# Kernel tuning notes

Hardware: AMD Instinct MI355X
Metric: run time of the kernel (lower is better)

Reference implementation:

```python
import jax, jax.numpy as jnp
import numpy as np


def setup_inputs() -> dict:
    key = jax.random.key(0)
    ks = jax.random.split(key, 5)
    shape = (8, 96, 128, 128)  # (N, C, H, W)
    X = jax.random.normal(ks[0], shape, dtype=jnp.float32)
    B = jax.random.uniform(ks[1], shape, dtype=jnp.float32)
    G1 = jax.random.uniform(ks[2], shape, dtype=jnp.float32)
    G2 = jax.random.uniform(ks[3], shape, dtype=jnp.float32)
    G3 = jax.random.uniform(ks[4], shape, dtype=jnp.float32)
    return {"X": X, "B": B, "G1": G1, "G2": G2, "G3": G3}


def _gaterecurrent(X, B, G1, G2, G3):
    # H[n,c,h,w] = B*X + G1*Hprev[h-1] + G2*Hprev[h] + G3*Hprev[h+1],
    # where Hprev is column w-1; column 0 has no recurrent input.
    # Scan over width; each carry is one column of shape (N, C, H).
    def to_cols(t):
        return jnp.moveaxis(t, -1, 0)  # (W, N, C, H)

    xs = tuple(to_cols(t) for t in (X, B, G1, G2, G3))
    n, c, h, w = X.shape
    h0 = jnp.zeros((n, c, h), dtype=X.dtype)
    zcol = jnp.zeros((n, c, 1), dtype=X.dtype)

    def step(h_prev, cols):
        x, b, g1, g2, g3 = cols
        h_up = jnp.concatenate([zcol, h_prev[..., :-1]], axis=-1)   # H[h-1, w-1]
        h_dn = jnp.concatenate([h_prev[..., 1:], zcol], axis=-1)    # H[h+1, w-1]
        h_new = b * x + g1 * h_up + g2 * h_prev + g3 * h_dn
        return h_new, h_new

    _, cols_out = jax.lax.scan(step, h0, xs)  # (W, N, C, H)
    return jnp.moveaxis(cols_out, 0, -1)      # (N, C, H, W)


def reference(X, B, G1, G2, G3):
    return _gaterecurrent(X, B, G1, G2, G3)
```

## Files before the change

kernel.cpp:

```cpp
#include <hip/hip_runtime.h>

#define HH 128
#define WW 128
#define SW 32

__global__ __launch_bounds__(128, 2) void gr2d_kernel(
    const float* __restrict__ X, const float* __restrict__ Bm,
    const float* __restrict__ G1, const float* __restrict__ G2,
    const float* __restrict__ G3, float* __restrict__ Out)
{
    const int t = threadIdx.x;
    const size_t rb = (size_t)blockIdx.x * (HH * WW) + (size_t)t * WW;

    __shared__ float halo[2][2];
    if (t == 0) { halo[0][0] = 0.f; halo[0][1] = 0.f; }
    __syncthreads();

    float hp = 0.f;

    for (int sw = 0; sw < WW / SW; ++sw) {
        const float* xp = X  + rb + sw * SW;
        const float* bp = Bm + rb + sw * SW;
        const float* ap = G1 + rb + sw * SW;
        const float* cp = G2 + rb + sw * SW;
        const float* dp = G3 + rb + sw * SW;

#define LDJ(p, j) (*reinterpret_cast<const float4*>((p) + 4 * (j)))
        float4 xv0 = LDJ(xp,0), xv1 = LDJ(xp,1), xv2 = LDJ(xp,2), xv3 = LDJ(xp,3),
               xv4 = LDJ(xp,4), xv5 = LDJ(xp,5), xv6 = LDJ(xp,6), xv7 = LDJ(xp,7);
        float4 bv0 = LDJ(bp,0), bv1 = LDJ(bp,1), bv2 = LDJ(bp,2), bv3 = LDJ(bp,3),
               bv4 = LDJ(bp,4), bv5 = LDJ(bp,5), bv6 = LDJ(bp,6), bv7 = LDJ(bp,7);
        float4 av0 = LDJ(ap,0), av1 = LDJ(ap,1), av2 = LDJ(ap,2), av3 = LDJ(ap,3),
               av4 = LDJ(ap,4), av5 = LDJ(ap,5), av6 = LDJ(ap,6), av7 = LDJ(ap,7);
        float4 cv0 = LDJ(cp,0), cv1 = LDJ(cp,1), cv2 = LDJ(cp,2), cv3 = LDJ(cp,3),
               cv4 = LDJ(cp,4), cv5 = LDJ(cp,5), cv6 = LDJ(cp,6), cv7 = LDJ(cp,7);
        float4 dv0 = LDJ(dp,0), dv1 = LDJ(dp,1), dv2 = LDJ(dp,2), dv3 = LDJ(dp,3),
               dv4 = LDJ(dp,4), dv5 = LDJ(dp,5), dv6 = LDJ(dp,6), dv7 = LDJ(dp,7);
        __builtin_amdgcn_sched_barrier(0);

#define MUL4(a, b) a.x *= b.x; a.y *= b.y; a.z *= b.z; a.w *= b.w;
        MUL4(xv0, bv0) MUL4(xv1, bv1) MUL4(xv2, bv2) MUL4(xv3, bv3)
        MUL4(xv4, bv4) MUL4(xv5, bv5) MUL4(xv6, bv6) MUL4(xv7, bv7)

#define STEP(xc, ac, cc, dc, par) do {                                      \
        float up = __shfl_up(hp, 1);                                        \
        float dn = __shfl_down(hp, 1);                                      \
        if (t == 63)  dn = halo[par][1];                                    \
        if (t == 64)  up = halo[par][0];                                    \
        if (t == 0)   up = 0.f;                                             \
        if (t == 127) dn = 0.f;                                             \
        const float h = xc + ac * up + cc * hp + dc * dn;                   \
        if (t == 63) halo[(par) ^ 1][0] = h;                                \
        if (t == 64) halo[(par) ^ 1][1] = h;                                \
        asm volatile("s_waitcnt lgkmcnt(0)" ::: "memory");                  \
        __builtin_amdgcn_s_barrier();                                       \
        hp = h; xc = h;                                                     \
    } while (0)

#define STEP4(v)                                                            \
        STEP(xv##v.x, av##v.x, cv##v.x, dv##v.x, 0);                        \
        STEP(xv##v.y, av##v.y, cv##v.y, dv##v.y, 1);                        \
        STEP(xv##v.z, av##v.z, cv##v.z, dv##v.z, 0);                        \
        STEP(xv##v.w, av##v.w, cv##v.w, dv##v.w, 1);

        STEP4(0) STEP4(1) STEP4(2) STEP4(3)
        STEP4(4) STEP4(5) STEP4(6) STEP4(7)

        float* op = Out + rb + sw * SW;
        *reinterpret_cast<float4*>(op + 0)  = xv0;
        *reinterpret_cast<float4*>(op + 4)  = xv1;
        *reinterpret_cast<float4*>(op + 8)  = xv2;
        *reinterpret_cast<float4*>(op + 12) = xv3;
        *reinterpret_cast<float4*>(op + 16) = xv4;
        *reinterpret_cast<float4*>(op + 20) = xv5;
        *reinterpret_cast<float4*>(op + 24) = xv6;
        *reinterpret_cast<float4*>(op + 28) = xv7;
    }
}

extern "C" void kernel_launch(void* const* d_in, const int* in_sizes, int n_in,
                              void* d_out, int out_size, void* d_ws, size_t ws_size,
                              hipStream_t stream) {
    const float* X  = (const float*)d_in[0];
    const float* Bm = (const float*)d_in[1];
    const float* G1 = (const float*)d_in[2];
    const float* G2 = (const float*)d_in[3];
    const float* G3 = (const float*)d_in[4];
    float* Out = (float*)d_out;

    const int planes = in_sizes[0] / (HH * WW);
    gr2d_kernel<<<dim3(planes), dim3(128), 0, stream>>>(X, Bm, G1, G2, G3, Out);
}
```

Measured before the change: 67.58 us.

## Double-buffer column loads with inline asm to overlap memory with scan

Replaces the sequential 32-column strip loop, which loaded and then scanned each strip, with a software pipeline over 16-column chunks. Two register buffers alternate: the next chunk's loads are issued through inline global_load asm before the current chunk is scanned, and vmcnt waits are counted by hand. The aim is to hide global memory latency behind the barrier-bound serial recurrence. The cost is hand-tracked vmcnt accounting, which is fragile because the stores are interleaved, and more registers held live for two buffers.

```diff
diff --git a/kernel.cpp b/kernel.cpp
--- a/kernel.cpp
+++ b/kernel.cpp
@@ -2,7 +2,68 @@
 
 #define HH 128
 #define WW 128
-#define SW 32
+
+typedef float f4 __attribute__((ext_vector_type(4)));
+
+#define GLOAD(dst, ptr, OFF)                                                  \
+    asm volatile("global_load_dwordx4 %0, %1, off offset:%2"                  \
+                 : "=&v"(dst) : "v"(ptr), "n"(OFF) : "memory");
+
+#define GSTORE(val, ptr, OFF)                                                 \
+    asm volatile("global_store_dwordx4 %0, %1, off offset:%2"                 \
+                 :: "v"(ptr), "v"(val), "n"(OFF) : "memory");
+
+#define VMCNT(N)                                                              \
+    asm volatile("s_waitcnt vmcnt(" #N ")" ::: "memory");                     \
+    __builtin_amdgcn_sched_barrier(0);
+
+#define LD4(P, s, ptr, WOFF)                                                  \
+    GLOAD(P##s##0, ptr, (WOFF)+0)   GLOAD(P##s##1, ptr, (WOFF)+16)            \
+    GLOAD(P##s##2, ptr, (WOFF)+32)  GLOAD(P##s##3, ptr, (WOFF)+48)
+
+#define LD20(P, WOFF)                                                         \
+    LD4(P, x, xp, WOFF) LD4(P, b, bp, WOFF) LD4(P, a, ap, WOFF)               \
+    LD4(P, c, cp, WOFF) LD4(P, d, dp, WOFF)
+
+#define ST4(P, WOFF)                                                          \
+    GSTORE(P##x0, op, (WOFF)+0)   GSTORE(P##x1, op, (WOFF)+16)                \
+    GSTORE(P##x2, op, (WOFF)+32)  GSTORE(P##x3, op, (WOFF)+48)
+
+#define DECLBUF(P)                                                            \
+    f4 P##x0,P##x1,P##x2,P##x3;                                               \
+    f4 P##b0,P##b1,P##b2,P##b3;                                               \
+    f4 P##a0,P##a1,P##a2,P##a3;                                               \
+    f4 P##c0,P##c1,P##c2,P##c3;                                               \
+    f4 P##d0,P##d1,P##d2,P##d3;
+
+#define MUL4(a, b)                                                            \
+    { (a)[0]*=(b)[0]; (a)[1]*=(b)[1]; (a)[2]*=(b)[2]; (a)[3]*=(b)[3]; }
+
+#define FUSE(P)                                                               \
+    MUL4(P##x0,P##b0) MUL4(P##x1,P##b1) MUL4(P##x2,P##b2) MUL4(P##x3,P##b3)
+
+#define STEP(xc, ac, cc, dc, par) do {                                        \
+        float up = __shfl_up(hp, 1);                                          \
+        float dn = __shfl_down(hp, 1);                                        \
+        if (t == 63)  dn = halo[par][1];                                      \
+        if (t == 64)  up = halo[par][0];                                      \
+        if (t == 0)   up = 0.f;                                               \
+        if (t == 127) dn = 0.f;                                               \
+        const float h = (xc) + (ac) * up + (cc) * hp + (dc) * dn;             \
+        if (t == 63) halo[(par) ^ 1][0] = h;                                  \
+        if (t == 64) halo[(par) ^ 1][1] = h;                                  \
+        asm volatile("s_waitcnt lgkmcnt(0)" ::: "memory");                    \
+        __builtin_amdgcn_s_barrier();                                         \
+        hp = h; (xc) = h;                                                     \
+    } while (0)
+
+#define STEP4(P, v)                                                           \
+    STEP(P##x##v[0], P##a##v[0], P##c##v[0], P##d##v[0], 0);                  \
+    STEP(P##x##v[1], P##a##v[1], P##c##v[1], P##d##v[1], 1);                  \
+    STEP(P##x##v[2], P##a##v[2], P##c##v[2], P##d##v[2], 0);                  \
+    STEP(P##x##v[3], P##a##v[3], P##c##v[3], P##d##v[3], 1);
+
+#define SCAN16(P) STEP4(P,0) STEP4(P,1) STEP4(P,2) STEP4(P,3)
 
 __global__ __launch_bounds__(128, 2) void gr2d_kernel(
     const float* __restrict__ X, const float* __restrict__ Bm,
@@ -11,71 +72,33 @@
 {
     const int t = threadIdx.x;
     const size_t rb = (size_t)blockIdx.x * (HH * WW) + (size_t)t * WW;
+    const float* xp = X  + rb;
+    const float* bp = Bm + rb;
+    const float* ap = G1 + rb;
+    const float* cp = G2 + rb;
+    const float* dp = G3 + rb;
+    float*       op = Out + rb;
 
     __shared__ float halo[2][2];
     if (t == 0) { halo[0][0] = 0.f; halo[0][1] = 0.f; }
     __syncthreads();
 
     float hp = 0.f;
+    DECLBUF(A)
+    DECLBUF(B)
 
-    for (int sw = 0; sw < WW / SW; ++sw) {
-        const float* xp = X  + rb + sw * SW;
-        const float* bp = Bm + rb + sw * SW;
-        const float* ap = G1 + rb + sw * SW;
-        const float* cp = G2 + rb + sw * SW;
-        const float* dp = G3 + rb + sw * SW;
+    LD20(A, 0)
 
-#define LDJ(p, j) (*reinterpret_cast<const float4*>((p) + 4 * (j)))
-        float4 xv0 = LDJ(xp,0), xv1 = LDJ(xp,1), xv2 = LDJ(xp,2), xv3 = LDJ(xp,3),
-               xv4 = LDJ(xp,4), xv5 = LDJ(xp,5), xv6 = LDJ(xp,6), xv7 = LDJ(xp,7);
-        float4 bv0 = LDJ(bp,0), bv1 = LDJ(bp,1), bv2 = LDJ(bp,2), bv3 = LDJ(bp,3),
-               bv4 = LDJ(bp,4), bv5 = LDJ(bp,5), bv6 = LDJ(bp,6), bv7 = LDJ(bp,7);
-        float4 av0 = LDJ(ap,0), av1 = LDJ(ap,1), av2 = LDJ(ap,2), av3 = LDJ(ap,3),
-               av4 = LDJ(ap,4), av5 = LDJ(ap,5), av6 = LDJ(ap,6), av7 = LDJ(ap,7);
-        float4 cv0 = LDJ(cp,0), cv1 = LDJ(cp,1), cv2 = LDJ(cp,2), cv3 = LDJ(cp,3),
-               cv4 = LDJ(cp,4), cv5 = LDJ(cp,5), cv6 = LDJ(cp,6), cv7 = LDJ(cp,7);
-        float4 dv0 = LDJ(dp,0), dv1 = LDJ(dp,1), dv2 = LDJ(dp,2), dv3 = LDJ(dp,3),
-               dv4 = LDJ(dp,4), dv5 = LDJ(dp,5), dv6 = LDJ(dp,6), dv7 = LDJ(dp,7);
-        __builtin_amdgcn_sched_barrier(0);
+    VMCNT(0)  LD20(B, 64)   FUSE(A) SCAN16(A) ST4(A, 0)
+    VMCNT(4)  LD20(A, 128)  FUSE(B) SCAN16(B) ST4(B, 64)
+    VMCNT(4)  LD20(B, 192)  FUSE(A) SCAN16(A) ST4(A, 128)
+    VMCNT(4)  LD20(A, 256)  FUSE(B) SCAN16(B) ST4(B, 192)
+    VMCNT(4)  LD20(B, 320)  FUSE(A) SCAN16(A) ST4(A, 256)
+    VMCNT(4)  LD20(A, 384)  FUSE(B) SCAN16(B) ST4(B, 320)
+    VMCNT(4)  LD20(B, 448)  FUSE(A) SCAN16(A) ST4(A, 384)
+    VMCNT(4)  FUSE(B) SCAN16(B) ST4(B, 448)
 
-#define MUL4(a, b) a.x *= b.x; a.y *= b.y; a.z *= b.z; a.w *= b.w;
-        MUL4(xv0, bv0) MUL4(xv1, bv1) MUL4(xv2, bv2) MUL4(xv3, bv3)
-        MUL4(xv4, bv4) MUL4(xv5, bv5) MUL4(xv6, bv6) MUL4(xv7, bv7)
-
-#define STEP(xc, ac, cc, dc, par) do {                                      \
-        float up = __shfl_up(hp, 1);                                        \
-        float dn = __shfl_down(hp, 1);                                      \
-        if (t == 63)  dn = halo[par][1];                                    \
-        if (t == 64)  up = halo[par][0];                                    \
-        if (t == 0)   up = 0.f;                                             \
-        if (t == 127) dn = 0.f;                                             \
-        const float h = xc + ac * up + cc * hp + dc * dn;                   \
-        if (t == 63) halo[(par) ^ 1][0] = h;                                \
-        if (t == 64) halo[(par) ^ 1][1] = h;                                \
-        asm volatile("s_waitcnt lgkmcnt(0)" ::: "memory");                  \
-        __builtin_amdgcn_s_barrier();                                       \
-        hp = h; xc = h;                                                     \
-    } while (0)
-
-#define STEP4(v)                                                            \
-        STEP(xv##v.x, av##v.x, cv##v.x, dv##v.x, 0);                        \
-        STEP(xv##v.y, av##v.y, cv##v.y, dv##v.y, 1);                        \
-        STEP(xv##v.z, av##v.z, cv##v.z, dv##v.z, 0);                        \
-        STEP(xv##v.w, av##v.w, cv##v.w, dv##v.w, 1);
-
-        STEP4(0) STEP4(1) STEP4(2) STEP4(3)
-        STEP4(4) STEP4(5) STEP4(6) STEP4(7)
-
-        float* op = Out + rb + sw * SW;
-        *reinterpret_cast<float4*>(op + 0)  = xv0;
-        *reinterpret_cast<float4*>(op + 4)  = xv1;
-        *reinterpret_cast<float4*>(op + 8)  = xv2;
-        *reinterpret_cast<float4*>(op + 12) = xv3;
-        *reinterpret_cast<float4*>(op + 16) = xv4;
-        *reinterpret_cast<float4*>(op + 20) = xv5;
-        *reinterpret_cast<float4*>(op + 24) = xv6;
-        *reinterpret_cast<float4*>(op + 28) = xv7;
-    }
+    asm volatile("s_waitcnt vmcnt(0)" ::: "memory");
 }
 
 extern "C" void kernel_launch(void* const* d_in, const int* in_sizes, int n_in,
```

Result: slower. 82.46 us (+22.0%).
